# Optimization experiments

Measured on AMD Instinct MI355X. Metric: run time of the kernel, lower is better.

The kernel has to match this reference:

```python
import jax, jax.numpy as jnp
import numpy as np

B, WAYS, SHOTS, C, H, W = 64, 10, 5, 128, 32, 32


def setup_inputs() -> dict:
    key = jax.random.key(0)
    k1, k2, k3 = jax.random.split(key, 3)
    q = jax.random.normal(k1, (B, C, H, W), dtype=jnp.float32)
    support = jax.random.normal(k2, (WAYS, SHOTS, C, H, W), dtype=jnp.float32)
    conv_w = jax.random.normal(k3, (H * W,), dtype=jnp.float32) * 0.03
    return {"q": q, "support": support, "conv_w": conv_w}


def reference(q, support, conv_w):
    b, c, h, w = q.shape
    ways, shots = support.shape[:2]
    hw = h * w
    # --- cal_covariance: per-class channel covariance ---
    # [ways, shots, C, h, w] -> [ways, C, shots*h*w]
    s = support.transpose(0, 2, 1, 3, 4).reshape(ways, c, shots * hw)
    s = s - s.mean(axis=2, keepdims=True)
    denom = jnp.float32(shots * hw - 1)
    cov = jnp.einsum('jcn,jdn->jcd', s, s) / denom  # [ways, C, C]
    # --- cal_similarity: per-pixel quadratic form diag(Q^T Sigma Q) ---
    qf = q.reshape(b, c, hw)
    qn = qf / jnp.linalg.norm(qf, axis=2, keepdims=True)  # L2 norm per channel row
    t = jnp.einsum('jcd,bdp->bjcp', cov, qn)              # [B, ways, C, hw]
    sim = jnp.einsum('bcp,bjcp->bjp', qn, t)              # diagonal only: [B, ways, hw]
    # --- classifier1: LeakyReLU(0.2) -> Dropout (eval identity) -> Conv1d(1,1,k=hw,stride=hw,bias=False) ---
    x = sim.reshape(b, ways * hw)
    x = jnp.where(x >= 0, x, 0.2 * x)
    out = jnp.einsum('bjp,p->bj', x.reshape(b, ways, hw), conv_w)  # [B, ways]
    return out
```

## Files before the change

### kernel.cpp

```cpp
#include <hip/hip_runtime.h>

typedef unsigned short u16;
typedef unsigned int u32;
typedef __attribute__((ext_vector_type(8))) short bf16x8;
typedef __attribute__((ext_vector_type(4))) short bf16x4v;
typedef __attribute__((ext_vector_type(4))) float f32x4;

#define NWAYS 10
#define NC 128
#define NHW 1024

__device__ __forceinline__ u16 f2bf(float f) {
  u32 u = __builtin_bit_cast(u32, f);
  return (u16)((u + 0x7fffu + ((u >> 16) & 1u)) >> 16);
}
__device__ __forceinline__ float bf2f(u16 h) {
  u32 u = ((u32)h) << 16;
  return __builtin_bit_cast(float, u);
}

__global__ __launch_bounds__(512) void k_phase1(const float* __restrict__ sup,
                                                const float* __restrict__ q,
                                                const float* __restrict__ cw,
                                                u16* __restrict__ Gpartb,
                                                float* __restrict__ mpart,
                                                u16* __restrict__ Wrawb,
                                                float* __restrict__ ss) {
  __shared__ u16 smem[NC * 256];
  __shared__ float saux[NC];
  int bid = blockIdx.x;
  int t = threadIdx.x;
  int w = t >> 6, l = t & 63, lr = l & 15, lg = l >> 4;

  if (bid < 200) {
    int j = bid / 20, chunk = bid % 20;
    int shot = chunk >> 2, p0 = (chunk & 3) * 256;
    const float* srcbase = sup + ((size_t)(j * 5 + shot) * NC) * NHW + p0;
#pragma unroll 4
    for (int it = 0; it < 16; ++it) {
      int c = it * 8 + w;
      int pos = t & 63;
      float4 v = *(const float4*)(srcbase + (size_t)c * NHW + pos * 4);
      int nl = pos * 4;
      int idx = c * 256 + (((nl >> 3) ^ (c & 15)) << 3) + (nl & 7);
      bf16x4v h;
      h[0] = (short)f2bf(v.x); h[1] = (short)f2bf(v.y);
      h[2] = (short)f2bf(v.z); h[3] = (short)f2bf(v.w);
      *(bf16x4v*)&smem[idx] = h;
      float s = v.x + v.y + v.z + v.w;
#pragma unroll
      for (int m = 1; m <= 32; m <<= 1) s += __shfl_xor(s, m, 64);
      if (l == 0) saux[c] = s;
    }
    __syncthreads();
    if (t < NC) mpart[(size_t)bid * NC + t] = saux[t];

    f32x4 acc[8];
#pragma unroll
    for (int bt = 0; bt < 8; ++bt) acc[bt] = (f32x4){0.f, 0.f, 0.f, 0.f};
#pragma unroll 1
    for (int kb = 0; kb < 8; ++kb) {
      int nn = kb * 32 + lg * 8;
      int arow = w * 16 + lr;
      bf16x8 fa = *(const bf16x8*)&smem[arow * 256 + (((nn >> 3) ^ (arow & 15)) << 3)];
      bf16x8 fb[8];
#pragma unroll
      for (int bt = 0; bt < 8; ++bt) {
        int drow = bt * 16 + lr;
        fb[bt] = *(const bf16x8*)&smem[drow * 256 + (((nn >> 3) ^ (drow & 15)) << 3)];
      }
#pragma unroll
      for (int bt = 0; bt < 8; ++bt)
        acc[bt] = __builtin_amdgcn_mfma_f32_16x16x32_bf16(fa, fb[bt], acc[bt], 0, 0, 0);
    }
    u16* gp = Gpartb + ((size_t)bid << 14);
#pragma unroll
    for (int bt = 0; bt < 8; ++bt)
#pragma unroll
      for (int r = 0; r < 4; ++r) {
        int cr = w * 16 + lg * 4 + r;
        int d = bt * 16 + lr;
        gp[cr * NC + d] = f2bf(acc[bt][r]);
      }
  } else {
    int bid2 = bid - 200;
    int b = bid2 >> 2, qr = bid2 & 3;
    u16* traw = smem;
    u16* twgt = smem + 16384;
    const float* base = q + (size_t)b * NC * NHW + qr * 256;
    const float* cwb = cw + qr * 256;

    float4 v[8];
    auto load_chunk = [&](int chunk) {
#pragma unroll
      for (int it = 0; it < 8; ++it) {
        int idx = it * 512 + t;
        int c = idx >> 5, pos = idx & 31;
        v[it] = *(const float4*)(base + (size_t)c * NHW + chunk * 128 + pos * 4);
      }
    };
    auto store_chunk = [&](int chunk) {
#pragma unroll
      for (int it = 0; it < 8; ++it) {
        int idx = it * 512 + t;
        int c = idx >> 5, pos = idx & 31;
        float4 vv = v[it];
        float4 wv = *(const float4*)(cwb + chunk * 128 + pos * 4);
        int nl = pos * 4;
        int off = c * 128 + (((nl >> 3) ^ (c & 15)) << 3) + (nl & 7);
        bf16x4v hr, hw;
        hr[0] = (short)f2bf(vv.x); hr[1] = (short)f2bf(vv.y);
        hr[2] = (short)f2bf(vv.z); hr[3] = (short)f2bf(vv.w);
        hw[0] = (short)f2bf(vv.x * wv.x); hw[1] = (short)f2bf(vv.y * wv.y);
        hw[2] = (short)f2bf(vv.z * wv.z); hw[3] = (short)f2bf(vv.w * wv.w);
        *(bf16x4v*)&traw[off] = hr;
        *(bf16x4v*)&twgt[off] = hw;
        float s = vv.x * vv.x + vv.y * vv.y + vv.z * vv.z + vv.w * vv.w;
#pragma unroll
        for (int m = 1; m <= 16; m <<= 1) s += __shfl_xor(s, m, 64);
        if ((l & 31) == 0) saux[c] += s;
      }
    };

    load_chunk(0);
    if (t < NC) saux[t] = 0.f;
    __syncthreads();
    store_chunk(0);
    __syncthreads();

    f32x4 acc[8];
#pragma unroll
    for (int bt = 0; bt < 8; ++bt) acc[bt] = (f32x4){0.f, 0.f, 0.f, 0.f};
#pragma unroll 1
    for (int chunk = 0; chunk < 2; ++chunk) {
      if (chunk < 1) load_chunk(1);
#pragma unroll
      for (int kb = 0; kb < 4; ++kb) {
        int nn = kb * 32 + lg * 8;
        int arow = w * 16 + lr;
        bf16x8 fa = *(const bf16x8*)&twgt[arow * 128 + (((nn >> 3) ^ (arow & 15)) << 3)];
        bf16x8 fb[8];
#pragma unroll
        for (int bt = 0; bt < 8; ++bt) {
          int drow = bt * 16 + lr;
          fb[bt] = *(const bf16x8*)&traw[drow * 128 + (((nn >> 3) ^ (drow & 15)) << 3)];
        }
#pragma unroll
        for (int bt = 0; bt < 8; ++bt)
          acc[bt] = __builtin_amdgcn_mfma_f32_16x16x32_bf16(fa, fb[bt], acc[bt], 0, 0, 0);
      }
      __syncthreads();
      if (chunk < 1) { store_chunk(1); __syncthreads(); }
    }

    if (t < NC) ss[(size_t)(qr * 64 + b) * NC + t] = saux[t];
    u16* wb = Wrawb + ((size_t)(qr * 64 + b) << 14);
#pragma unroll
    for (int bt = 0; bt < 8; ++bt)
#pragma unroll
      for (int r = 0; r < 4; ++r) {
        int cr = w * 16 + lg * 4 + r;
        int d = bt * 16 + lr;
        wb[cr * NC + d] = f2bf(acc[bt][r]);
      }
  }
}

__global__ __launch_bounds__(256) void k_fin(const u16* __restrict__ Gpartb,
                                             const float* __restrict__ mpart,
                                             u16* __restrict__ covb,
                                             float* __restrict__ out) {
  __shared__ float msd[NC];
  int j = blockIdx.x >> 4, rg = blockIdx.x & 15;
  int t = threadIdx.x;
  if (blockIdx.x < 3) {
    int o = blockIdx.x * 256 + t;
    if (o < 64 * NWAYS) out[o] = 0.f;
  }
  if (t < NC) {
    float s = 0.f;
#pragma unroll
    for (int k = 0; k < 20; ++k) s += mpart[(size_t)(j * 20 + k) * NC + t];
    msd[t] = s;
  }
  __syncthreads();
  int e = rg * 1024 + t * 4;
  int c = e >> 7, d0 = e & 127;
  float g[4] = {0.f, 0.f, 0.f, 0.f};
#pragma unroll
  for (int k = 0; k < 20; ++k) {
    bf16x4v v = *(const bf16x4v*)(Gpartb + (((size_t)(j * 20 + k)) << 14) + e);
#pragma unroll
    for (int r = 0; r < 4; ++r) g[r] += bf2f((u16)v[r]);
  }
  bf16x4v o;
#pragma unroll
  for (int r = 0; r < 4; ++r)
    o[r] = (short)f2bf((g[r] - msd[c] * msd[d0 + r] * (1.0f / 5120.0f)) * (1.0f / 5119.0f));
  *(bf16x4v*)(covb + (((size_t)j) << 14) + e) = o;
}

__global__ __launch_bounds__(256) void k_wndot(const u16* __restrict__ Wrawb,
                                               const float* __restrict__ ss,
                                               const u16* __restrict__ covb,
                                               float* __restrict__ out) {
  __shared__ float rnl[NC];
  __shared__ float red[4 * NWAYS];
  int b = blockIdx.x >> 2, rg = blockIdx.x & 3;
  int t = threadIdx.x;
  int w = t >> 6, l = t & 63;
  if (t < NC) {
    float s = 0.f;
#pragma unroll
    for (int qr = 0; qr < 4; ++qr) s += ss[(size_t)(qr * 64 + b) * NC + t];
    rnl[t] = rsqrtf(s);
  }
  __syncthreads();
  int e = rg * 4096 + t * 16;
  int c = e >> 7, d0 = e & 127;
  float wn[16];
#pragma unroll
  for (int k = 0; k < 16; ++k) wn[k] = 0.f;
#pragma unroll
  for (int qr = 0; qr < 4; ++qr) {
    const u16* src = Wrawb + (((size_t)(qr * 64 + b)) << 14) + e;
    bf16x8 v0 = *(const bf16x8*)src;
    bf16x8 v1 = *(const bf16x8*)(src + 8);
#pragma unroll
    for (int k = 0; k < 8; ++k) { wn[k] += bf2f((u16)v0[k]); wn[8 + k] += bf2f((u16)v1[k]); }
  }
  float rc = rnl[c];
#pragma unroll
  for (int k = 0; k < 16; ++k) wn[k] *= rc * rnl[d0 + k];

  float acc[NWAYS];
#pragma unroll
  for (int j = 0; j < NWAYS; ++j) {
    const u16* cj = covb + ((size_t)j << 14) + e;
    bf16x8 c0 = *(const bf16x8*)cj;
    bf16x8 c1 = *(const bf16x8*)(cj + 8);
    float s = 0.f;
#pragma unroll
    for (int k = 0; k < 8; ++k) s += wn[k] * bf2f((u16)c0[k]) + wn[8 + k] * bf2f((u16)c1[k]);
    acc[j] = s;
  }
#pragma unroll
  for (int j = 0; j < NWAYS; ++j)
#pragma unroll
    for (int m = 1; m <= 32; m <<= 1) acc[j] += __shfl_xor(acc[j], m, 64);
  if (l == 0)
#pragma unroll
    for (int j = 0; j < NWAYS; ++j) red[w * NWAYS + j] = acc[j];
  __syncthreads();
  if (t < NWAYS)
    atomicAdd(&out[b * NWAYS + t],
              red[t] + red[NWAYS + t] + red[2 * NWAYS + t] + red[3 * NWAYS + t]);
}

extern "C" void kernel_launch(void* const* d_in, const int* in_sizes, int n_in,
                              void* d_out, int out_size, void* d_ws, size_t ws_size,
                              hipStream_t stream) {
  (void)in_sizes; (void)n_in; (void)out_size; (void)ws_size;
  const float* q = (const float*)d_in[0];
  const float* sup = (const float*)d_in[1];
  const float* cw = (const float*)d_in[2];
  float* out = (float*)d_out;

  char* p = (char*)d_ws;
  u16* Gpartb = (u16*)p;    p += (size_t)200 * 16384 * 2;
  float* mpart = (float*)p; p += (size_t)200 * 128 * 4;
  u16* covb = (u16*)p;      p += (size_t)10 * 16384 * 2;
  u16* Wrawb = (u16*)p;     p += (size_t)256 * 16384 * 2;
  float* ssb = (float*)p;

  k_phase1<<<456, 512, 0, stream>>>(sup, q, cw, Gpartb, mpart, Wrawb, ssb);
  k_fin<<<160, 256, 0, stream>>>(Gpartb, mpart, covb, out);
  k_wndot<<<256, 256, 0, stream>>>(Wrawb, ssb, covb, out);
}
```

Before: 36.68 us.

## Fuse three kernels into one persistent kernel with grid barriers

Merges the phase1, covariance-finalize and weighted-dot kernels into a single launch of 456 blocks, separated by atomic-counter grid barriers. This removes two kernel launch gaps and the separate zeroing of the output, and the final stage writes the output directly instead of using atomicAdd. Each final-stage block now handles a whole batch row with 8 waves rather than splitting it across 4 blocks. The cost is the barrier spin latency, fewer active blocks in the later stages, and a requirement that all 456 blocks are co-resident; if they are not, the barrier deadlocks.

After: 137.1 us. +273.8%, slower.

```diff
diff --git a/kernel.cpp b/kernel.cpp
--- a/kernel.cpp
+++ b/kernel.cpp
@@ -9,6 +9,7 @@
 #define NWAYS 10
 #define NC 128
 #define NHW 1024
+#define NBLK 456
 
 __device__ __forceinline__ u16 f2bf(float f) {
   u32 u = __builtin_bit_cast(u32, f);
@@ -19,18 +20,38 @@
   return __builtin_bit_cast(float, u);
 }
 
-__global__ __launch_bounds__(512) void k_phase1(const float* __restrict__ sup,
+__device__ __forceinline__ void grid_barrier(u32* cnt, u32 base, int t) {
+  __syncthreads();
+  if (t == 0) {
+    __threadfence();
+    atomicAdd(cnt, 1u);
+    while ((u32)(atomicAdd(cnt, 0u) - base) < (u32)NBLK) __builtin_amdgcn_s_sleep(8);
+    __threadfence();
+  }
+  __syncthreads();
+}
+
+__global__ __launch_bounds__(512, 4) void k_all(const float* __restrict__ sup,
                                                 const float* __restrict__ q,
                                                 const float* __restrict__ cw,
                                                 u16* __restrict__ Gpartb,
                                                 float* __restrict__ mpart,
                                                 u16* __restrict__ Wrawb,
-                                                float* __restrict__ ss) {
+                                                float* __restrict__ ss,
+                                                u16* __restrict__ covb,
+                                                float* __restrict__ out,
+                                                u32* __restrict__ bar) {
   __shared__ u16 smem[NC * 256];
   __shared__ float saux[NC];
+  __shared__ float red[8 * NWAYS];
   int bid = blockIdx.x;
   int t = threadIdx.x;
   int w = t >> 6, l = t & 63, lr = l & 15, lg = l >> 4;
+  u32 base0 = 0, base1 = 0;
+  if (t == 0) {
+    base0 = atomicAdd(&bar[0], 0u);
+    base1 = atomicAdd(&bar[1], 0u);
+  }
 
   if (bid < 200) {
     int j = bid / 20, chunk = bid % 20;
@@ -164,97 +185,92 @@
         wb[cr * NC + d] = f2bf(acc[bt][r]);
       }
   }
-}
-
-__global__ __launch_bounds__(256) void k_fin(const u16* __restrict__ Gpartb,
-                                             const float* __restrict__ mpart,
-                                             u16* __restrict__ covb,
-                                             float* __restrict__ out) {
-  __shared__ float msd[NC];
-  int j = blockIdx.x >> 4, rg = blockIdx.x & 15;
-  int t = threadIdx.x;
-  if (blockIdx.x < 3) {
-    int o = blockIdx.x * 256 + t;
-    if (o < 64 * NWAYS) out[o] = 0.f;
-  }
-  if (t < NC) {
-    float s = 0.f;
-#pragma unroll
-    for (int k = 0; k < 20; ++k) s += mpart[(size_t)(j * 20 + k) * NC + t];
-    msd[t] = s;
-  }
-  __syncthreads();
-  int e = rg * 1024 + t * 4;
-  int c = e >> 7, d0 = e & 127;
-  float g[4] = {0.f, 0.f, 0.f, 0.f};
-#pragma unroll
-  for (int k = 0; k < 20; ++k) {
-    bf16x4v v = *(const bf16x4v*)(Gpartb + (((size_t)(j * 20 + k)) << 14) + e);
-#pragma unroll
-    for (int r = 0; r < 4; ++r) g[r] += bf2f((u16)v[r]);
-  }
-  bf16x4v o;
-#pragma unroll
-  for (int r = 0; r < 4; ++r)
-    o[r] = (short)f2bf((g[r] - msd[c] * msd[d0 + r] * (1.0f / 5120.0f)) * (1.0f / 5119.0f));
-  *(bf16x4v*)(covb + (((size_t)j) << 14) + e) = o;
-}
-
-__global__ __launch_bounds__(256) void k_wndot(const u16* __restrict__ Wrawb,
-                                               const float* __restrict__ ss,
-                                               const u16* __restrict__ covb,
-                                               float* __restrict__ out) {
-  __shared__ float rnl[NC];
-  __shared__ float red[4 * NWAYS];
-  int b = blockIdx.x >> 2, rg = blockIdx.x & 3;
-  int t = threadIdx.x;
-  int w = t >> 6, l = t & 63;
-  if (t < NC) {
-    float s = 0.f;
-#pragma unroll
-    for (int qr = 0; qr < 4; ++qr) s += ss[(size_t)(qr * 64 + b) * NC + t];
-    rnl[t] = rsqrtf(s);
-  }
-  __syncthreads();
-  int e = rg * 4096 + t * 16;
-  int c = e >> 7, d0 = e & 127;
-  float wn[16];
-#pragma unroll
-  for (int k = 0; k < 16; ++k) wn[k] = 0.f;
-#pragma unroll
-  for (int qr = 0; qr < 4; ++qr) {
-    const u16* src = Wrawb + (((size_t)(qr * 64 + b)) << 14) + e;
-    bf16x8 v0 = *(const bf16x8*)src;
-    bf16x8 v1 = *(const bf16x8*)(src + 8);
-#pragma unroll
-    for (int k = 0; k < 8; ++k) { wn[k] += bf2f((u16)v0[k]); wn[8 + k] += bf2f((u16)v1[k]); }
-  }
-  float rc = rnl[c];
-#pragma unroll
-  for (int k = 0; k < 16; ++k) wn[k] *= rc * rnl[d0 + k];
-
-  float acc[NWAYS];
-#pragma unroll
-  for (int j = 0; j < NWAYS; ++j) {
-    const u16* cj = covb + ((size_t)j << 14) + e;
-    bf16x8 c0 = *(const bf16x8*)cj;
-    bf16x8 c1 = *(const bf16x8*)(cj + 8);
-    float s = 0.f;
-#pragma unroll
-    for (int k = 0; k < 8; ++k) s += wn[k] * bf2f((u16)c0[k]) + wn[8 + k] * bf2f((u16)c1[k]);
-    acc[j] = s;
-  }
-#pragma unroll
-  for (int j = 0; j < NWAYS; ++j)
-#pragma unroll
-    for (int m = 1; m <= 32; m <<= 1) acc[j] += __shfl_xor(acc[j], m, 64);
-  if (l == 0)
-#pragma unroll
-    for (int j = 0; j < NWAYS; ++j) red[w * NWAYS + j] = acc[j];
-  __syncthreads();
-  if (t < NWAYS)
-    atomicAdd(&out[b * NWAYS + t],
-              red[t] + red[NWAYS + t] + red[2 * NWAYS + t] + red[3 * NWAYS + t]);
+
+  grid_barrier(&bar[0], base0, t);
+
+  if (bid < 80) {
+    int j = bid >> 3, sub = bid & 7;
+    if (t < NC) {
+      float s = 0.f;
+#pragma unroll
+      for (int k = 0; k < 20; ++k) s += mpart[(size_t)(j * 20 + k) * NC + t];
+      saux[t] = s;
+    }
+    __syncthreads();
+    int e = sub * 2048 + t * 4;
+    int c = e >> 7, d0 = e & 127;
+    float g[4] = {0.f, 0.f, 0.f, 0.f};
+#pragma unroll
+    for (int k = 0; k < 20; ++k) {
+      bf16x4v v = *(const bf16x4v*)(Gpartb + (((size_t)(j * 20 + k)) << 14) + e);
+#pragma unroll
+      for (int r = 0; r < 4; ++r) g[r] += bf2f((u16)v[r]);
+    }
+    bf16x4v o;
+#pragma unroll
+    for (int r = 0; r < 4; ++r)
+      o[r] = (short)f2bf((g[r] - saux[c] * saux[d0 + r] * (1.0f / 5120.0f)) * (1.0f / 5119.0f));
+    *(bf16x4v*)(covb + (((size_t)j) << 14) + e) = o;
+  }
+
+  grid_barrier(&bar[1], base1, t);
+
+  if (bid < 64) {
+    int b = bid;
+    if (t < NC) {
+      float s = 0.f;
+#pragma unroll
+      for (int qr = 0; qr < 4; ++qr) s += ss[(size_t)(qr * 64 + b) * NC + t];
+      saux[t] = rsqrtf(s);
+    }
+    __syncthreads();
+    int e = t * 32;
+    int c = e >> 7, d0 = e & 127;
+    float wn[32];
+#pragma unroll
+    for (int k = 0; k < 32; ++k) wn[k] = 0.f;
+#pragma unroll
+    for (int qr = 0; qr < 4; ++qr) {
+      const u16* src = Wrawb + (((size_t)(qr * 64 + b)) << 14) + e;
+#pragma unroll
+      for (int h = 0; h < 4; ++h) {
+        bf16x8 v8 = *(const bf16x8*)(src + h * 8);
+#pragma unroll
+        for (int k = 0; k < 8; ++k) wn[h * 8 + k] += bf2f((u16)v8[k]);
+      }
+    }
+    float rc = saux[c];
+#pragma unroll
+    for (int k = 0; k < 32; ++k) wn[k] *= rc * saux[d0 + k];
+
+    float acc[NWAYS];
+#pragma unroll
+    for (int j = 0; j < NWAYS; ++j) {
+      const u16* cj = covb + ((size_t)j << 14) + e;
+      float s = 0.f;
+#pragma unroll
+      for (int h = 0; h < 4; ++h) {
+        bf16x8 c8 = *(const bf16x8*)(cj + h * 8);
+#pragma unroll
+        for (int k = 0; k < 8; ++k) s += wn[h * 8 + k] * bf2f((u16)c8[k]);
+      }
+      acc[j] = s;
+    }
+#pragma unroll
+    for (int j = 0; j < NWAYS; ++j)
+#pragma unroll
+      for (int m = 1; m <= 32; m <<= 1) acc[j] += __shfl_xor(acc[j], m, 64);
+    if (l == 0)
+#pragma unroll
+      for (int j = 0; j < NWAYS; ++j) red[w * NWAYS + j] = acc[j];
+    __syncthreads();
+    if (t < NWAYS) {
+      float s = 0.f;
+#pragma unroll
+      for (int wv = 0; wv < 8; ++wv) s += red[wv * NWAYS + t];
+      out[b * NWAYS + t] = s;
+    }
+  }
 }
 
 extern "C" void kernel_launch(void* const* d_in, const int* in_sizes, int n_in,
@@ -271,9 +287,8 @@
   float* mpart = (float*)p; p += (size_t)200 * 128 * 4;
   u16* covb = (u16*)p;      p += (size_t)10 * 16384 * 2;
   u16* Wrawb = (u16*)p;     p += (size_t)256 * 16384 * 2;
-  float* ssb = (float*)p;
-
-  k_phase1<<<456, 512, 0, stream>>>(sup, q, cw, Gpartb, mpart, Wrawb, ssb);
-  k_fin<<<160, 256, 0, stream>>>(Gpartb, mpart, covb, out);
-  k_wndot<<<256, 256, 0, stream>>>(Wrawb, ssb, covb, out);
-}
+  float* ssb = (float*)p;   p += (size_t)256 * 128 * 4;
+  u32* bar = (u32*)p;
+
+  k_all<<<NBLK, 512, 0, stream>>>(sup, q, cw, Gpartb, mpart, Wrawb, ssb, covb, out, bar);
+}
```

## Fuse covariance finalize and weighted dot into one kernel, zero output in phase1

Applied to the files above, without the earlier changes.

Merges the covariance-finalize kernel and the per-batch weighted-dot kernel into a single launch. Each block recomputes its 16-row slice of one class covariance from the partial Grams and applies it directly to 16 batches, so the bf16 covariance buffer is never written or re-read. Output zeroing moves into the first kernel. This drops one kernel launch and one global round-trip, but Wrawb is now re-read once per class (ten times) and the covariance partials are reduced redundantly across batch-quarter blocks.

New measurement: 49.20 us. +34.1%, slower.

```diff
diff --git a/kernel.cpp b/kernel.cpp
--- a/kernel.cpp
+++ b/kernel.cpp
@@ -25,7 +25,8 @@
                                                 u16* __restrict__ Gpartb,
                                                 float* __restrict__ mpart,
                                                 u16* __restrict__ Wrawb,
-                                                float* __restrict__ ss) {
+                                                float* __restrict__ ss,
+                                                float* __restrict__ out) {
   __shared__ u16 smem[NC * 256];
   __shared__ float saux[NC];
   int bid = blockIdx.x;
@@ -84,6 +85,10 @@
       }
   } else {
     int bid2 = bid - 200;
+    if (bid2 < 2) {
+      int o = bid2 * 512 + t;
+      if (o < 64 * NWAYS) out[o] = 0.f;
+    }
     int b = bid2 >> 2, qr = bid2 & 3;
     u16* traw = smem;
     u16* twgt = smem + 16384;
@@ -166,95 +171,82 @@
   }
 }
 
-__global__ __launch_bounds__(256) void k_fin(const u16* __restrict__ Gpartb,
-                                             const float* __restrict__ mpart,
-                                             u16* __restrict__ covb,
-                                             float* __restrict__ out) {
+__global__ __launch_bounds__(512) void k_fin2(const u16* __restrict__ Gpartb,
+                                              const float* __restrict__ mpart,
+                                              const u16* __restrict__ Wrawb,
+                                              const float* __restrict__ ss,
+                                              float* __restrict__ out) {
   __shared__ float msd[NC];
-  int j = blockIdx.x >> 4, rg = blockIdx.x & 15;
+  __shared__ float rnl[16 * NC];
+  __shared__ float red[8 * 16];
+  int bid = blockIdx.x;
+  int j = bid >> 5, sub = (bid >> 2) & 7, bq = bid & 3;
   int t = threadIdx.x;
-  if (blockIdx.x < 3) {
-    int o = blockIdx.x * 256 + t;
-    if (o < 64 * NWAYS) out[o] = 0.f;
-  }
+  int w = t >> 6, l = t & 63;
+
   if (t < NC) {
     float s = 0.f;
 #pragma unroll
     for (int k = 0; k < 20; ++k) s += mpart[(size_t)(j * 20 + k) * NC + t];
     msd[t] = s;
   }
+  {
+    int idx = t * 4;
+    int bb = idx >> 7;
+    int b = bq * 16 + bb;
+    int c0 = idx & 127;
+    float4 s4 = (float4){0.f, 0.f, 0.f, 0.f};
+#pragma unroll
+    for (int qr = 0; qr < 4; ++qr) {
+      float4 v = *(const float4*)(ss + (size_t)(qr * 64 + b) * NC + c0);
+      s4.x += v.x; s4.y += v.y; s4.z += v.z; s4.w += v.w;
+    }
+    rnl[idx] = rsqrtf(s4.x); rnl[idx + 1] = rsqrtf(s4.y);
+    rnl[idx + 2] = rsqrtf(s4.z); rnl[idx + 3] = rsqrtf(s4.w);
+  }
   __syncthreads();
-  int e = rg * 1024 + t * 4;
-  int c = e >> 7, d0 = e & 127;
-  float g[4] = {0.f, 0.f, 0.f, 0.f};
-#pragma unroll
-  for (int k = 0; k < 20; ++k) {
-    bf16x4v v = *(const bf16x4v*)(Gpartb + (((size_t)(j * 20 + k)) << 14) + e);
-#pragma unroll
-    for (int r = 0; r < 4; ++r) g[r] += bf2f((u16)v[r]);
-  }
-  bf16x4v o;
-#pragma unroll
-  for (int r = 0; r < 4; ++r)
-    o[r] = (short)f2bf((g[r] - msd[c] * msd[d0 + r] * (1.0f / 5120.0f)) * (1.0f / 5119.0f));
-  *(bf16x4v*)(covb + (((size_t)j) << 14) + e) = o;
-}
-
-__global__ __launch_bounds__(256) void k_wndot(const u16* __restrict__ Wrawb,
-                                               const float* __restrict__ ss,
-                                               const u16* __restrict__ covb,
-                                               float* __restrict__ out) {
-  __shared__ float rnl[NC];
-  __shared__ float red[4 * NWAYS];
-  int b = blockIdx.x >> 2, rg = blockIdx.x & 3;
-  int t = threadIdx.x;
-  int w = t >> 6, l = t & 63;
-  if (t < NC) {
+
+  int r = t >> 5, d0 = (t & 31) * 4;
+  int c = sub * 16 + r;
+  float cv[4];
+  {
+    float g[4] = {0.f, 0.f, 0.f, 0.f};
+#pragma unroll
+    for (int k = 0; k < 20; ++k) {
+      bf16x4v v = *(const bf16x4v*)(Gpartb + (((size_t)(j * 20 + k)) << 14) + c * NC + d0);
+#pragma unroll
+      for (int i = 0; i < 4; ++i) g[i] += bf2f((u16)v[i]);
+    }
+#pragma unroll
+    for (int i = 0; i < 4; ++i)
+      cv[i] = (g[i] - msd[c] * msd[d0 + i] * (1.0f / 5120.0f)) * (1.0f / 5119.0f);
+  }
+
+#pragma unroll 1
+  for (int bb = 0; bb < 16; ++bb) {
+    int b = bq * 16 + bb;
+    float rnrow = rnl[bb * NC + c];
+    float4 rd = *(const float4*)&rnl[bb * NC + d0];
+    float ws[4] = {0.f, 0.f, 0.f, 0.f};
+#pragma unroll
+    for (int qr = 0; qr < 4; ++qr) {
+      bf16x4v wv = *(const bf16x4v*)(Wrawb + (((size_t)(qr * 64 + b)) << 14) + c * NC + d0);
+#pragma unroll
+      for (int i = 0; i < 4; ++i) ws[i] += bf2f((u16)wv[i]);
+    }
+    float s = rnrow * (cv[0] * rd.x * ws[0] + cv[1] * rd.y * ws[1] +
+                       cv[2] * rd.z * ws[2] + cv[3] * rd.w * ws[3]);
+#pragma unroll
+    for (int m = 1; m <= 32; m <<= 1) s += __shfl_xor(s, m, 64);
+    if (l == 0) red[w * 16 + bb] = s;
+  }
+  __syncthreads();
+  if (t < 16) {
     float s = 0.f;
 #pragma unroll
-    for (int qr = 0; qr < 4; ++qr) s += ss[(size_t)(qr * 64 + b) * NC + t];
-    rnl[t] = rsqrtf(s);
-  }
-  __syncthreads();
-  int e = rg * 4096 + t * 16;
-  int c = e >> 7, d0 = e & 127;
-  float wn[16];
-#pragma unroll
-  for (int k = 0; k < 16; ++k) wn[k] = 0.f;
-#pragma unroll
-  for (int qr = 0; qr < 4; ++qr) {
-    const u16* src = Wrawb + (((size_t)(qr * 64 + b)) << 14) + e;
-    bf16x8 v0 = *(const bf16x8*)src;
-    bf16x8 v1 = *(const bf16x8*)(src + 8);
-#pragma unroll
-    for (int k = 0; k < 8; ++k) { wn[k] += bf2f((u16)v0[k]); wn[8 + k] += bf2f((u16)v1[k]); }
-  }
-  float rc = rnl[c];
-#pragma unroll
-  for (int k = 0; k < 16; ++k) wn[k] *= rc * rnl[d0 + k];
-
-  float acc[NWAYS];
-#pragma unroll
-  for (int j = 0; j < NWAYS; ++j) {
-    const u16* cj = covb + ((size_t)j << 14) + e;
-    bf16x8 c0 = *(const bf16x8*)cj;
-    bf16x8 c1 = *(const bf16x8*)(cj + 8);
-    float s = 0.f;
-#pragma unroll
-    for (int k = 0; k < 8; ++k) s += wn[k] * bf2f((u16)c0[k]) + wn[8 + k] * bf2f((u16)c1[k]);
-    acc[j] = s;
-  }
-#pragma unroll
-  for (int j = 0; j < NWAYS; ++j)
-#pragma unroll
-    for (int m = 1; m <= 32; m <<= 1) acc[j] += __shfl_xor(acc[j], m, 64);
-  if (l == 0)
-#pragma unroll
-    for (int j = 0; j < NWAYS; ++j) red[w * NWAYS + j] = acc[j];
-  __syncthreads();
-  if (t < NWAYS)
-    atomicAdd(&out[b * NWAYS + t],
-              red[t] + red[NWAYS + t] + red[2 * NWAYS + t] + red[3 * NWAYS + t]);
+    for (int wv = 0; wv < 8; ++wv) s += red[wv * 16 + t];
+    atomicAdd(&out[(bq * 16 + t) * NWAYS + j], s);
+  }
 }
 
 extern "C" void kernel_launch(void* const* d_in, const int* in_sizes, int n_in,
@@ -269,11 +261,9 @@
   char* p = (char*)d_ws;
   u16* Gpartb = (u16*)p;    p += (size_t)200 * 16384 * 2;
   float* mpart = (float*)p; p += (size_t)200 * 128 * 4;
-  u16* covb = (u16*)p;      p += (size_t)10 * 16384 * 2;
   u16* Wrawb = (u16*)p;     p += (size_t)256 * 16384 * 2;
   float* ssb = (float*)p;
 
-  k_phase1<<<456, 512, 0, stream>>>(sup, q, cw, Gpartb, mpart, Wrawb, ssb);
-  k_fin<<<160, 256, 0, stream>>>(Gpartb, mpart, covb, out);
-  k_wndot<<<256, 256, 0, stream>>>(Wrawb, ssb, covb, out);
-}
+  k_phase1<<<456, 512, 0, stream>>>(sup, q, cw, Gpartb, mpart, Wrawb, ssb, out);
+  k_fin2<<<320, 512, 0, stream>>>(Gpartb, mpart, Wrawb, ssb, out);
+}
```

## Halve phase-1 block count by doubling per-block reduction length

Applied to the files above, without the earlier changes.

Each phase-1 block now reduces twice as many pixels: support blocks cover 512 pixels in two sub-tiles and query blocks cover 512 pixels in four chunks. The grid drops from 456 to 228 blocks. This halves the bf16 partial Gram and W matrices written to the workspace and later re-read by the finalize and dot kernels. Zeroing of the output moves from the finalize kernel into phase 1. The cost is fewer blocks than compute units on a 256-CU part and longer serial work per block, so latency hiding and occupancy may suffer.

Measured after the change: 36.06 us. Within noise of the previous version (-1.7%).

```diff
diff --git a/kernel.cpp b/kernel.cpp
--- a/kernel.cpp
+++ b/kernel.cpp
@@ -25,54 +25,62 @@
                                                 u16* __restrict__ Gpartb,
                                                 float* __restrict__ mpart,
                                                 u16* __restrict__ Wrawb,
-                                                float* __restrict__ ss) {
+                                                float* __restrict__ ss,
+                                                float* __restrict__ out) {
   __shared__ u16 smem[NC * 256];
   __shared__ float saux[NC];
   int bid = blockIdx.x;
   int t = threadIdx.x;
   int w = t >> 6, l = t & 63, lr = l & 15, lg = l >> 4;
 
-  if (bid < 200) {
-    int j = bid / 20, chunk = bid % 20;
-    int shot = chunk >> 2, p0 = (chunk & 3) * 256;
+  if (bid < 100) {
+    int j = bid / 10, chunk = bid % 10;
+    int shot = chunk >> 1, p0 = (chunk & 1) * 512;
     const float* srcbase = sup + ((size_t)(j * 5 + shot) * NC) * NHW + p0;
+    if (t < NC) saux[t] = 0.f;
+    __syncthreads();
+
+    f32x4 acc[8];
+#pragma unroll
+    for (int bt = 0; bt < 8; ++bt) acc[bt] = (f32x4){0.f, 0.f, 0.f, 0.f};
+
+#pragma unroll 1
+    for (int sub = 0; sub < 2; ++sub) {
+      const float* srcsub = srcbase + sub * 256;
 #pragma unroll 4
-    for (int it = 0; it < 16; ++it) {
-      int c = it * 8 + w;
-      int pos = t & 63;
-      float4 v = *(const float4*)(srcbase + (size_t)c * NHW + pos * 4);
-      int nl = pos * 4;
-      int idx = c * 256 + (((nl >> 3) ^ (c & 15)) << 3) + (nl & 7);
-      bf16x4v h;
-      h[0] = (short)f2bf(v.x); h[1] = (short)f2bf(v.y);
-      h[2] = (short)f2bf(v.z); h[3] = (short)f2bf(v.w);
-      *(bf16x4v*)&smem[idx] = h;
-      float s = v.x + v.y + v.z + v.w;
-#pragma unroll
-      for (int m = 1; m <= 32; m <<= 1) s += __shfl_xor(s, m, 64);
-      if (l == 0) saux[c] = s;
+      for (int it = 0; it < 16; ++it) {
+        int c = it * 8 + w;
+        float4 v = *(const float4*)(srcsub + (size_t)c * NHW + l * 4);
+        int nl = l * 4;
+        int idx = c * 256 + (((nl >> 3) ^ (c & 15)) << 3) + (nl & 7);
+        bf16x4v h;
+        h[0] = (short)f2bf(v.x); h[1] = (short)f2bf(v.y);
+        h[2] = (short)f2bf(v.z); h[3] = (short)f2bf(v.w);
+        *(bf16x4v*)&smem[idx] = h;
+        float s = v.x + v.y + v.z + v.w;
+#pragma unroll
+        for (int m = 1; m <= 32; m <<= 1) s += __shfl_xor(s, m, 64);
+        if (l == 0) saux[c] += s;
+      }
+      __syncthreads();
+#pragma unroll
+      for (int kb = 0; kb < 8; ++kb) {
+        int nn = kb * 32 + lg * 8;
+        int arow = w * 16 + lr;
+        bf16x8 fa = *(const bf16x8*)&smem[arow * 256 + (((nn >> 3) ^ (arow & 15)) << 3)];
+        bf16x8 fb[8];
+#pragma unroll
+        for (int bt = 0; bt < 8; ++bt) {
+          int drow = bt * 16 + lr;
+          fb[bt] = *(const bf16x8*)&smem[drow * 256 + (((nn >> 3) ^ (drow & 15)) << 3)];
+        }
+#pragma unroll
+        for (int bt = 0; bt < 8; ++bt)
+          acc[bt] = __builtin_amdgcn_mfma_f32_16x16x32_bf16(fa, fb[bt], acc[bt], 0, 0, 0);
+      }
+      __syncthreads();
     }
-    __syncthreads();
     if (t < NC) mpart[(size_t)bid * NC + t] = saux[t];
-
-    f32x4 acc[8];
-#pragma unroll
-    for (int bt = 0; bt < 8; ++bt) acc[bt] = (f32x4){0.f, 0.f, 0.f, 0.f};
-#pragma unroll 1
-    for (int kb = 0; kb < 8; ++kb) {
-      int nn = kb * 32 + lg * 8;
-      int arow = w * 16 + lr;
-      bf16x8 fa = *(const bf16x8*)&smem[arow * 256 + (((nn >> 3) ^ (arow & 15)) << 3)];
-      bf16x8 fb[8];
-#pragma unroll
-      for (int bt = 0; bt < 8; ++bt) {
-        int drow = bt * 16 + lr;
-        fb[bt] = *(const bf16x8*)&smem[drow * 256 + (((nn >> 3) ^ (drow & 15)) << 3)];
-      }
-#pragma unroll
-      for (int bt = 0; bt < 8; ++bt)
-        acc[bt] = __builtin_amdgcn_mfma_f32_16x16x32_bf16(fa, fb[bt], acc[bt], 0, 0, 0);
-    }
     u16* gp = Gpartb + ((size_t)bid << 14);
 #pragma unroll
     for (int bt = 0; bt < 8; ++bt)
@@ -83,12 +91,16 @@
         gp[cr * NC + d] = f2bf(acc[bt][r]);
       }
   } else {
-    int bid2 = bid - 200;
-    int b = bid2 >> 2, qr = bid2 & 3;
+    int bid2 = bid - 100;
+    if (bid2 < 2) {
+      int o = bid2 * 512 + t;
+      if (o < 64 * NWAYS) out[o] = 0.f;
+    }
+    int b = bid2 >> 1, half = bid2 & 1;
     u16* traw = smem;
     u16* twgt = smem + 16384;
-    const float* base = q + (size_t)b * NC * NHW + qr * 256;
-    const float* cwb = cw + qr * 256;
+    const float* base = q + (size_t)b * NC * NHW + half * 512;
+    const float* cwb = cw + half * 512;
 
     float4 v[8];
     auto load_chunk = [&](int chunk) {
@@ -132,8 +144,8 @@
 #pragma unroll
     for (int bt = 0; bt < 8; ++bt) acc[bt] = (f32x4){0.f, 0.f, 0.f, 0.f};
 #pragma unroll 1
-    for (int chunk = 0; chunk < 2; ++chunk) {
-      if (chunk < 1) load_chunk(1);
+    for (int chunk = 0; chunk < 4; ++chunk) {
+      if (chunk < 3) load_chunk(chunk + 1);
 #pragma unroll
       for (int kb = 0; kb < 4; ++kb) {
         int nn = kb * 32 + lg * 8;
@@ -150,11 +162,11 @@
           acc[bt] = __builtin_amdgcn_mfma_f32_16x16x32_bf16(fa, fb[bt], acc[bt], 0, 0, 0);
       }
       __syncthreads();
-      if (chunk < 1) { store_chunk(1); __syncthreads(); }
+      if (chunk < 3) { store_chunk(chunk + 1); __syncthreads(); }
     }
 
-    if (t < NC) ss[(size_t)(qr * 64 + b) * NC + t] = saux[t];
-    u16* wb = Wrawb + ((size_t)(qr * 64 + b) << 14);
+    if (t < NC) ss[(size_t)(half * 64 + b) * NC + t] = saux[t];
+    u16* wb = Wrawb + ((size_t)(half * 64 + b) << 14);
 #pragma unroll
     for (int bt = 0; bt < 8; ++bt)
 #pragma unroll
@@ -168,19 +180,14 @@
 
 __global__ __launch_bounds__(256) void k_fin(const u16* __restrict__ Gpartb,
                                              const float* __restrict__ mpart,
-                                             u16* __restrict__ covb,
-                                             float* __restrict__ out) {
+                                             u16* __restrict__ covb) {
   __shared__ float msd[NC];
   int j = blockIdx.x >> 4, rg = blockIdx.x & 15;
   int t = threadIdx.x;
-  if (blockIdx.x < 3) {
-    int o = blockIdx.x * 256 + t;
-    if (o < 64 * NWAYS) out[o] = 0.f;
-  }
   if (t < NC) {
     float s = 0.f;
 #pragma unroll
-    for (int k = 0; k < 20; ++k) s += mpart[(size_t)(j * 20 + k) * NC + t];
+    for (int k = 0; k < 10; ++k) s += mpart[(size_t)(j * 10 + k) * NC + t];
     msd[t] = s;
   }
   __syncthreads();
@@ -188,8 +195,8 @@
   int c = e >> 7, d0 = e & 127;
   float g[4] = {0.f, 0.f, 0.f, 0.f};
 #pragma unroll
-  for (int k = 0; k < 20; ++k) {
-    bf16x4v v = *(const bf16x4v*)(Gpartb + (((size_t)(j * 20 + k)) << 14) + e);
+  for (int k = 0; k < 10; ++k) {
+    bf16x4v v = *(const bf16x4v*)(Gpartb + (((size_t)(j * 10 + k)) << 14) + e);
 #pragma unroll
     for (int r = 0; r < 4; ++r) g[r] += bf2f((u16)v[r]);
   }
@@ -210,9 +217,7 @@
   int t = threadIdx.x;
   int w = t >> 6, l = t & 63;
   if (t < NC) {
-    float s = 0.f;
-#pragma unroll
-    for (int qr = 0; qr < 4; ++qr) s += ss[(size_t)(qr * 64 + b) * NC + t];
+    float s = ss[(size_t)b * NC + t] + ss[(size_t)(64 + b) * NC + t];
     rnl[t] = rsqrtf(s);
   }
   __syncthreads();
@@ -222,7 +227,7 @@
 #pragma unroll
   for (int k = 0; k < 16; ++k) wn[k] = 0.f;
 #pragma unroll
-  for (int qr = 0; qr < 4; ++qr) {
+  for (int qr = 0; qr < 2; ++qr) {
     const u16* src = Wrawb + (((size_t)(qr * 64 + b)) << 14) + e;
     bf16x8 v0 = *(const bf16x8*)src;
     bf16x8 v1 = *(const bf16x8*)(src + 8);
@@ -267,13 +272,13 @@
   float* out = (float*)d_out;
 
   char* p = (char*)d_ws;
-  u16* Gpartb = (u16*)p;    p += (size_t)200 * 16384 * 2;
-  float* mpart = (float*)p; p += (size_t)200 * 128 * 4;
+  u16* Gpartb = (u16*)p;    p += (size_t)100 * 16384 * 2;
+  float* mpart = (float*)p; p += (size_t)100 * 128 * 4;
   u16* covb = (u16*)p;      p += (size_t)10 * 16384 * 2;
-  u16* Wrawb = (u16*)p;     p += (size_t)256 * 16384 * 2;
+  u16* Wrawb = (u16*)p;     p += (size_t)128 * 16384 * 2;
   float* ssb = (float*)p;
 
-  k_phase1<<<456, 512, 0, stream>>>(sup, q, cw, Gpartb, mpart, Wrawb, ssb);
-  k_fin<<<160, 256, 0, stream>>>(Gpartb, mpart, covb, out);
+  k_phase1<<<228, 512, 0, stream>>>(sup, q, cw, Gpartb, mpart, Wrawb, ssb, out);
+  k_fin<<<160, 256, 0, stream>>>(Gpartb, mpart, covb);
   k_wndot<<<256, 256, 0, stream>>>(Wrawb, ssb, covb, out);
 }
```
